# Kernel optimization log

Hardware: AMD Instinct MI355X
Metric: run time of the kernel (lower is better)

The kernel has to match this reference:

```python
import jax, jax.numpy as jnp
import numpy as np

HEADS = 8
DIM_HEAD = 32
TOP_K = 256
KMEANS_ITERS = 10
EPS_LN = 1e-6
EPS_L2 = 1e-12


def chan_layer_norm(x, gamma, beta):
    # x: (b, c, L); normalize across channel dim (biased variance)
    mean = jnp.mean(x, axis=1, keepdims=True)
    var = jnp.var(x, axis=1, keepdims=True)
    return gamma * (x - mean) / (jnp.sqrt(var) + EPS_LN) + beta


def l2norm_ch(t):
    # F.normalize(t, dim=1): L2-normalize over channel axis of (B, c, L)
    n = jnp.linalg.norm(t, axis=1, keepdims=True)
    return t / jnp.maximum(n, EPS_L2)


def conv1x1(x, w):
    # x: (b, c_in, L), w: (c_out, c_in)  -> (b, c_out, L)
    return jnp.einsum('oc,bcl->bol', w, x)


def _dist2(x, c):
    # squared L2 distances, x: (N, d), c: (k, d) -> (N, k)
    return (jnp.sum(x * x, -1, keepdims=True)
            - 2.0 * x @ c.T
            + jnp.sum(c * c, -1)[None, :])


def kmeans_fit(x, k, iters):
    # Lloyd's algorithm, deterministic init = first k points
    c0 = x[:k]

    def step(c, _):
        assign = jnp.argmin(_dist2(x, c), axis=-1)           # (N,)
        sums = jax.ops.segment_sum(x, assign, num_segments=k)
        cnts = jax.ops.segment_sum(jnp.ones((x.shape[0],), x.dtype), assign,
                                   num_segments=k)
        new_c = jnp.where(cnts[:, None] > 0,
                          sums / jnp.maximum(cnts, 1.0)[:, None], c)
        return new_c, None

    c, _ = jax.lax.scan(step, c0, None, length=iters)
    return c


def select_best_ind(q, k, v, top_k):
    # q: (B, Lq, d), k/v: (B, Lk, d); B = b*heads
    B, Lk, d = k.shape
    q_flat = q.reshape(-1, d)
    centroids = kmeans_fit(q_flat, top_k, KMEANS_ITERS)       # (top_k, d)
    k_flat = k.reshape(-1, d)
    k_cluster = jnp.argmin(_dist2(k_flat, centroids), axis=-1).reshape(B, Lk)
    k_centers = centroids[k_cluster]                          # (B, Lk, d)
    k_dist = jnp.sum(jnp.abs(k_centers - k), axis=-1)         # (B, Lk)
    _, best_k = jax.lax.top_k(k_dist, top_k)                  # largest dists
    idx = best_k[:, :, None]
    k_sel = jnp.take_along_axis(k, idx, axis=1)
    v_sel = jnp.take_along_axis(v, idx, axis=1)
    return k_sel, v_sel


def reference(query_source, context, w_q, w_kv, w_out,
              ln_ctx_gamma, ln_ctx_beta, ln_q_gamma, ln_q_beta,
              ln_out_gamma, ln_out_beta, gamma_scale):
    b, c, L_query = query_source.shape
    ctx = chan_layer_norm(context, ln_ctx_gamma, ln_ctx_beta)
    qs = chan_layer_norm(query_source, ln_q_gamma, ln_q_beta)

    kv = conv1x1(ctx, w_kv)                                   # (b, 2*inner, Lc)
    k, v = jnp.split(kv, 2, axis=1)
    q = conv1x1(qs, w_q)                                      # (b, inner, Lq)

    def fold(t):  # b (h c) L -> (b h) c L
        B, hc, L = t.shape
        return t.reshape(B, HEADS, DIM_HEAD, L).reshape(B * HEADS, DIM_HEAD, L)

    q, k, v = fold(q), fold(k), fold(v)
    q, k = l2norm_ch(q), l2norm_ch(k)
    # b d L -> b L d
    q = jnp.swapaxes(q, 1, 2)
    k = jnp.swapaxes(k, 1, 2)
    v = jnp.swapaxes(v, 1, 2)

    k, v = select_best_ind(q, k, v, TOP_K)

    sim = jnp.einsum('bid,bjd->bij', q, k)                    # (b*h, Lq, top_k)
    attn = jax.nn.softmax(sim, axis=-1)
    out = jnp.einsum('bij,bjd->bid', attn, v)                 # (b*h, Lq, dh)

    out = out.reshape(b, HEADS, L_query, DIM_HEAD)
    out = jnp.transpose(out, (0, 1, 3, 2)).reshape(b, HEADS * DIM_HEAD, L_query)
    out = conv1x1(out, w_out)
    out = chan_layer_norm(out, ln_out_gamma, ln_out_beta)
    return gamma_scale[0] * out + query_source


def setup_inputs() -> dict:
    key = jax.random.key(0)
    ks = jax.random.split(key, 8)
    dim, inner = 256, HEADS * DIM_HEAD
    b, Lq, Lc = 2, 4096, 4096
    inp = {
        'query_source': jax.random.normal(ks[0], (b, dim, Lq), jnp.float32),
        'context': jax.random.normal(ks[1], (b, dim, Lc), jnp.float32),
        'w_q': jax.random.normal(ks[2], (inner, dim), jnp.float32) * 0.05,
        'w_kv': jax.random.normal(ks[3], (2 * inner, dim), jnp.float32) * 0.05,
        'w_out': jax.random.normal(ks[4], (dim, inner), jnp.float32) * 0.05,
        'ln_ctx_gamma': jnp.ones((1, dim, 1), jnp.float32),
        'ln_ctx_beta': jnp.zeros((1, dim, 1), jnp.float32),
        'ln_q_gamma': jnp.ones((1, dim, 1), jnp.float32),
        'ln_q_beta': jnp.zeros((1, dim, 1), jnp.float32),
        'ln_out_gamma': jnp.ones((1, dim, 1), jnp.float32),
        'ln_out_beta': jnp.zeros((1, dim, 1), jnp.float32),
        'gamma_scale': jax.random.normal(ks[5], (1,), jnp.float32),
    }
    return inp
```

## Files before the change

### kernel.cpp

```cpp
#include <hip/hip_runtime.h>
#include <math.h>

#define CDIM 256
#define LSEQ 4096
#define NBH 16
#define NPTS 65536
#define KC 256

__device__ __forceinline__ float fadd(float a, float b){ return __fadd_rn(a,b); }
__device__ __forceinline__ float fmul(float a, float b){ return __fmul_rn(a,b); }
__device__ __forceinline__ float fsub(float a, float b){ return __fsub_rn(a,b); }

__device__ __forceinline__ float sum32_np(const float* e){
    float l[16];
    #pragma unroll
    for (int j = 0; j < 16; j++) l[j] = fadd(e[j], e[j + 16]);
    float t3[8];
    #pragma unroll
    for (int j = 0; j < 8; j++) t3[j] = fadd(l[j], l[j + 8]);
    float t6[4];
    #pragma unroll
    for (int j = 0; j < 4; j++) t6[j] = fadd(t3[j], t3[j + 4]);
    return fadd(fadd(t6[0], t6[2]), fadd(t6[1], t6[3]));
}

__global__ __launch_bounds__(64) void ln_np(const float* __restrict__ x,
        const float* __restrict__ g, const float* __restrict__ bt,
        float* __restrict__ y) {
    int gid = blockIdx.x * 64 + threadIdx.x;
    int b = gid >> 12, l = gid & 4095;
    const float* xb = x + (size_t)b * CDIM * LSEQ + l;
    float s = 0.f;
    #pragma unroll 8
    for (int c = 0; c < 256; c++) s = fadd(s, xb[(size_t)c * LSEQ]);
    float mean = __fdiv_rn(s, 256.f);
    float s2 = 0.f;
    #pragma unroll 8
    for (int c = 0; c < 256; c++) {
        float d = fsub(xb[(size_t)c * LSEQ], mean);
        s2 = fadd(s2, fmul(d, d));
    }
    float var = __fdiv_rn(s2, 256.f);
    float den = fadd(__fsqrt_rn(var), 1e-6f);
    float* yb = y + (size_t)b * CDIM * LSEQ + l;
    #pragma unroll 4
    for (int c = 0; c < 256; c++) {
        float d = fsub(xb[(size_t)c * LSEQ], mean);
        yb[(size_t)c * LSEQ] = fadd(__fdiv_rn(fmul(g[c], d), den), bt[c]);
    }
}

template<int COT, int NL>
__global__ __launch_bounds__(256) void conv_nl(const float* __restrict__ W, int wrow0,
        const float* __restrict__ X, float* __restrict__ Y, int nrows) {
    __shared__ float ws[COT * 256];
    int tid = threadIdx.x;
    int l0 = blockIdx.x * (256 * NL) + tid;
    int o0 = blockIdx.y * COT;
    int b = blockIdx.z;
    {
        const float4* wb4 = (const float4*)(W + (size_t)(wrow0 + o0) * CDIM);
        float4* ws4 = (float4*)ws;
        for (int i = tid; i < COT * 64; i += 256) ws4[i] = wb4[i];
    }
    __syncthreads();
    const float* xb = X + (size_t)b * CDIM * LSEQ;
    float acc[COT][NL];
    #pragma unroll
    for (int oo = 0; oo < COT; oo++)
        #pragma unroll
        for (int i = 0; i < NL; i++) acc[oo][i] = 0.f;
    const float4* ws4 = (const float4*)ws;
    for (int c = 0; c < 256; c += 4) {
        float xv[NL][4];
        #pragma unroll
        for (int i = 0; i < NL; i++) {
            #pragma unroll
            for (int k = 0; k < 4; k++)
                xv[i][k] = xb[(size_t)(c + k) * LSEQ + l0 + i * 256];
        }
        #pragma unroll
        for (int oo = 0; oo < COT; oo++) {
            float4 w = ws4[(oo * 256 + c) >> 2];
            #pragma unroll
            for (int i = 0; i < NL; i++) {
                acc[oo][i] = fadd(acc[oo][i], fmul(w.x, xv[i][0]));
                acc[oo][i] = fadd(acc[oo][i], fmul(w.y, xv[i][1]));
                acc[oo][i] = fadd(acc[oo][i], fmul(w.z, xv[i][2]));
                acc[oo][i] = fadd(acc[oo][i], fmul(w.w, xv[i][3]));
            }
        }
    }
    #pragma unroll
    for (int oo = 0; oo < COT; oo++)
        #pragma unroll
        for (int i = 0; i < NL; i++)
            Y[((size_t)b * nrows + o0 + oo) * LSEQ + l0 + i * 256] = acc[oo][i];
}

__global__ __launch_bounds__(256) void fold_np(const float* __restrict__ src,
        int srcRows, int row0, int donorm, float* __restrict__ dst,
        float* __restrict__ xxout, float* __restrict__ centout,
        float* __restrict__ ccout) {
    int p = blockIdx.x * 256 + threadIdx.x;
    int bh = p >> 12, l = p & 4095;
    int b = bh >> 3, h = bh & 7;
    const float* sp = src + ((size_t)b * srcRows + row0 + h * 32) * LSEQ + l;
    float x[32];
    #pragma unroll
    for (int t = 0; t < 32; t++) x[t] = sp[(size_t)t * LSEQ];
    float4* dp4 = (float4*)(dst + (size_t)p * 32);
    if (donorm) {
        float ss = 0.f;
        #pragma unroll
        for (int t = 0; t < 32; t++) ss = fadd(ss, fmul(x[t], x[t]));
        float n = __fsqrt_rn(ss);
        float den = fmaxf(n, 1e-12f);
        #pragma unroll
        for (int t = 0; t < 32; t++) x[t] = __fdiv_rn(x[t], den);
    }
    #pragma unroll
    for (int t = 0; t < 8; t++)
        dp4[t] = make_float4(x[4*t], x[4*t+1], x[4*t+2], x[4*t+3]);
    if (xxout) {
        float e[32];
        #pragma unroll
        for (int t = 0; t < 32; t++) e[t] = fmul(x[t], x[t]);
        float xv = sum32_np(e);
        xxout[p] = xv;
        if (centout && p < KC) {
            float4* cp4 = (float4*)(centout + (size_t)p * 32);
            #pragma unroll
            for (int t = 0; t < 8; t++)
                cp4[t] = make_float4(x[4*t], x[4*t+1], x[4*t+2], x[4*t+3]);
            ccout[p] = xv;
        }
    }
}

__global__ __launch_bounds__(256) void assign4p(const float* __restrict__ pts,
        const float* __restrict__ xx, const float* __restrict__ cent,
        const float* __restrict__ cc, int* __restrict__ asn, int* __restrict__ hist) {
    __shared__ float sc[8192];
    __shared__ float scc[256];
    __shared__ int bins[256];
    int tid = threadIdx.x, c = blockIdx.x;
    {
        const float4* c4 = (const float4*)cent;
        float4* s4 = (float4*)sc;
        for (int i = tid; i < 2048; i += 256) s4[i] = c4[i];
    }
    scc[tid] = cc[tid];
    bins[tid] = 0;
    __syncthreads();
    int pg = tid >> 2, quarter = tid & 3;
    int pb = c * 256 + pg * 4;
    float x[4][32];
    float xp[4];
    #pragma unroll
    for (int i = 0; i < 4; i++) {
        const float4* pp = (const float4*)(pts + (size_t)(pb + i) * 32);
        #pragma unroll
        for (int t = 0; t < 8; t++) {
            float4 f = pp[t];
            x[i][4*t] = f.x; x[i][4*t+1] = f.y; x[i][4*t+2] = f.z; x[i][4*t+3] = f.w;
        }
        xp[i] = xx[pb + i];
    }
    float bd[4] = {3.4e38f, 3.4e38f, 3.4e38f, 3.4e38f};
    int bj[4] = {0, 0, 0, 0};
    int jbase = quarter * 64;
    for (int jj = 0; jj < 64; jj++) {
        int j = jbase + jj;
        const float4* cj = (const float4*)(sc + j * 32);
        float w[32];
        #pragma unroll
        for (int t = 0; t < 8; t++) {
            float4 f = cj[t];
            w[4*t] = f.x; w[4*t+1] = f.y; w[4*t+2] = f.z; w[4*t+3] = f.w;
        }
        float sj = scc[j];
        #pragma unroll
        for (int i = 0; i < 4; i++) {
            float g = 0.f;
            #pragma unroll
            for (int t = 0; t < 32; t++) g = __builtin_fmaf(x[i][t], w[t], g);
            float d = fadd(fsub(xp[i], fmul(2.f, g)), sj);
            if (d < bd[i]) { bd[i] = d; bj[i] = j; }
        }
    }
    #pragma unroll
    for (int i = 0; i < 4; i++) {
        float ob; int oj;
        ob = __shfl_xor(bd[i], 1); oj = __shfl_xor(bj[i], 1);
        if (ob < bd[i]) { bd[i] = ob; bj[i] = oj; }
        ob = __shfl_xor(bd[i], 2); oj = __shfl_xor(bj[i], 2);
        if (ob < bd[i]) { bd[i] = ob; bj[i] = oj; }
    }
    if (quarter == 0) {
        #pragma unroll
        for (int i = 0; i < 4; i++) {
            asn[pb + i] = bj[i];
            atomicAdd(&bins[bj[i]], 1);
        }
    }
    __syncthreads();
    hist[c * 256 + tid] = bins[tid];
}

__global__ __launch_bounds__(256) void scan_chunks(const int* __restrict__ hist,
        int* __restrict__ chunkbase, int* __restrict__ totals) {
    __shared__ int a[256];
    int j = blockIdx.x, c = threadIdx.x;
    a[c] = hist[(size_t)c * 256 + j];
    __syncthreads();
    for (int d = 1; d < 256; d <<= 1) {
        int v = a[c];
        int u = (c >= d) ? a[c - d] : 0;
        __syncthreads();
        a[c] = v + u;
        __syncthreads();
    }
    chunkbase[(size_t)c * 256 + j] = (c == 0) ? 0 : a[c - 1];
    if (c == 255) totals[j] = a[255];
}

__global__ __launch_bounds__(256) void scatter_v5(const int* __restrict__ asn,
        const int* __restrict__ chunkbase, const int* __restrict__ totals,
        int* __restrict__ perm) {
    __shared__ int cb[256];
    __shared__ int al[256];
    int c = blockIdx.x, tid = threadIdx.x;
    cb[tid] = totals[tid];
    al[tid] = asn[c * 256 + tid];
    __syncthreads();
    for (int d = 1; d < 256; d <<= 1) {
        int v = cb[tid];
        int u = (tid >= d) ? cb[tid - d] : 0;
        __syncthreads();
        cb[tid] = v + u;
        __syncthreads();
    }
    int my = al[tid];
    int base = (my == 0) ? 0 : cb[my - 1];
    int r = 0;
    for (int i = 0; i < tid; i++) r += (al[i] == my) ? 1 : 0;
    perm[base + chunkbase[(size_t)c * 256 + my] + r] = c * 256 + tid;
}

#define STILE 128
__global__ __launch_bounds__(256) void sumk_v4(const float* __restrict__ pts,
        const int* __restrict__ perm, const int* __restrict__ totals,
        float* __restrict__ cent, float* __restrict__ cc) {
    __shared__ int cb[256];
    __shared__ float buf[2][STILE][32];
    int j = blockIdx.x, tid = threadIdx.x;
    cb[tid] = totals[tid];
    __syncthreads();
    for (int d = 1; d < 256; d <<= 1) {
        int v = cb[tid];
        int u = (tid >= d) ? cb[tid - d] : 0;
        __syncthreads();
        cb[tid] = v + u;
        __syncthreads();
    }
    int base = (j == 0) ? 0 : cb[j - 1];
    int n = totals[j];
    int t = tid & 31, r0 = tid >> 5;
    for (int r = r0; r < STILE; r += 8) {
        if (r < n) buf[0][r][t] = pts[(size_t)perm[base + r] * 32 + t];
    }
    __syncthreads();
    float s = 0.f;
    int b = 0;
    for (int i0 = 0; i0 < n; i0 += STILE, b ^= 1) {
        int nx = i0 + STILE;
        if (nx < n) {
            for (int r = r0; r < STILE; r += 8) {
                int g = nx + r;
                if (g < n) buf[b ^ 1][r][t] = pts[(size_t)perm[base + g] * 32 + t];
            }
        }
        if (tid < 32) {
            int m = n - i0; if (m > STILE) m = STILE;
            int i = 0;
            for (; i + 4 <= m; i += 4) {
                s = fadd(s, buf[b][i][tid]);
                s = fadd(s, buf[b][i + 1][tid]);
                s = fadd(s, buf[b][i + 2][tid]);
                s = fadd(s, buf[b][i + 3][tid]);
            }
            for (; i < m; i++) s = fadd(s, buf[b][i][tid]);
        }
        __syncthreads();
    }
    if (tid < 32) {
        float v;
        if (n > 0) {
            v = __fdiv_rn(s, (float)n);
            cent[(size_t)j * 32 + tid] = v;
        } else {
            v = cent[(size_t)j * 32 + tid];
        }
        float e = fmul(v, v);
        e = fadd(e, __shfl_xor(e, 16));
        e = fadd(e, __shfl_xor(e, 8));
        e = fadd(e, __shfl_xor(e, 4));
        e = fadd(e, __shfl_xor(e, 2));
        e = fadd(e, __shfl_xor(e, 1));
        if (tid == 0) cc[j] = e;
    }
}

__global__ __launch_bounds__(256) void kdist4p(const float* __restrict__ pts,
        const float* __restrict__ cent, const float* __restrict__ cc,
        float* __restrict__ kd) {
    __shared__ float sc[8192];
    __shared__ float scc[256];
    int tid = threadIdx.x, c = blockIdx.x;
    {
        const float4* c4 = (const float4*)cent;
        float4* s4 = (float4*)sc;
        for (int i = tid; i < 2048; i += 256) s4[i] = c4[i];
    }
    scc[tid] = cc[tid];
    __syncthreads();
    int pg = tid >> 2, quarter = tid & 3;
    int pb = c * 256 + pg * 4;
    float x[4][32];
    float xp[4];
    #pragma unroll
    for (int i = 0; i < 4; i++) {
        const float4* pp = (const float4*)(pts + (size_t)(pb + i) * 32);
        #pragma unroll
        for (int t = 0; t < 8; t++) {
            float4 f = pp[t];
            x[i][4*t] = f.x; x[i][4*t+1] = f.y; x[i][4*t+2] = f.z; x[i][4*t+3] = f.w;
        }
        float e[32];
        #pragma unroll
        for (int t = 0; t < 32; t++) e[t] = fmul(x[i][t], x[i][t]);
        xp[i] = sum32_np(e);
    }
    float bd[4] = {3.4e38f, 3.4e38f, 3.4e38f, 3.4e38f};
    int bj[4] = {0, 0, 0, 0};
    int jbase = quarter * 64;
    for (int jj = 0; jj < 64; jj++) {
        int j = jbase + jj;
        const float4* cj = (const float4*)(sc + j * 32);
        float w[32];
        #pragma unroll
        for (int t = 0; t < 8; t++) {
            float4 f = cj[t];
            w[4*t] = f.x; w[4*t+1] = f.y; w[4*t+2] = f.z; w[4*t+3] = f.w;
        }
        float sj = scc[j];
        #pragma unroll
        for (int i = 0; i < 4; i++) {
            float g = 0.f;
            #pragma unroll
            for (int t = 0; t < 32; t++) g = __builtin_fmaf(x[i][t], w[t], g);
            float d = fadd(fsub(xp[i], fmul(2.f, g)), sj);
            if (d < bd[i]) { bd[i] = d; bj[i] = j; }
        }
    }
    #pragma unroll
    for (int i = 0; i < 4; i++) {
        float ob; int oj;
        ob = __shfl_xor(bd[i], 1); oj = __shfl_xor(bj[i], 1);
        if (ob < bd[i]) { bd[i] = ob; bj[i] = oj; }
        ob = __shfl_xor(bd[i], 2); oj = __shfl_xor(bj[i], 2);
        if (ob < bd[i]) { bd[i] = ob; bj[i] = oj; }
    }
    if (quarter == 0) {
        #pragma unroll
        for (int i = 0; i < 4; i++) {
            const float* cb = &sc[bj[i] * 32];
            float e[32];
            #pragma unroll
            for (int t = 0; t < 32; t++) e[t] = fabsf(fsub(cb[t], x[i][t]));
            kd[pb + i] = sum32_np(e);
        }
    }
}

__global__ __launch_bounds__(256) void topk_v2(const float* __restrict__ kd,
        const float* __restrict__ k_t, const float* __restrict__ v_t,
        float* __restrict__ ksel, float* __restrict__ vsel) {
    __shared__ unsigned uv[4096];
    __shared__ int hist[256];
    __shared__ unsigned s_prefix;
    __shared__ int s_rem;
    __shared__ int sc1[256];
    __shared__ int out_src[256];
    int bh = blockIdx.x, tid = threadIdx.x;
    for (int i = tid; i < 4096; i += 256) uv[i] = __float_as_uint(kd[bh * 4096 + i]);
    if (tid == 0) { s_prefix = 0u; s_rem = 256; }
    out_src[tid] = 0;
    __syncthreads();
    for (int pass = 0; pass < 4; pass++) {
        int shift = 24 - 8 * pass;
        hist[tid] = 0;
        __syncthreads();
        unsigned pfx = s_prefix;
        for (int i = tid; i < 4096; i += 256) {
            unsigned u = uv[i];
            bool in = (pass == 0) || ((u >> (shift + 8)) == (pfx >> (shift + 8)));
            if (in) atomicAdd(&hist[(u >> shift) & 255], 1);
        }
        __syncthreads();
        if (tid == 0) {
            int rem = s_rem, cum = 0, b;
            for (b = 255; b >= 0; b--) {
                if (cum + hist[b] >= rem) break;
                cum += hist[b];
            }
            s_rem = rem - cum;
            s_prefix = s_prefix | ((unsigned)b << shift);
        }
        __syncthreads();
    }
    unsigned T = s_prefix;
    int r = s_rem;
    int base_i = tid * 16;
    int ec = 0;
    for (int q = 0; q < 16; q++) ec += (uv[base_i + q] == T) ? 1 : 0;
    sc1[tid] = ec;
    __syncthreads();
    for (int d = 1; d < 256; d <<= 1) {
        int t0 = sc1[tid];
        int u0 = (tid >= d) ? sc1[tid - d] : 0;
        __syncthreads();
        sc1[tid] = t0 + u0;
        __syncthreads();
    }
    int erank = (tid == 0) ? 0 : sc1[tid - 1];
    __syncthreads();
    bool incl[16];
    int ic = 0;
    for (int q = 0; q < 16; q++) {
        unsigned u = uv[base_i + q];
        bool inc;
        if (u > T) inc = true;
        else if (u == T) { inc = (erank < r); erank++; }
        else inc = false;
        incl[q] = inc;
        ic += inc ? 1 : 0;
    }
    sc1[tid] = ic;
    __syncthreads();
    for (int d = 1; d < 256; d <<= 1) {
        int t0 = sc1[tid];
        int u0 = (tid >= d) ? sc1[tid - d] : 0;
        __syncthreads();
        sc1[tid] = t0 + u0;
        __syncthreads();
    }
    int pos = (tid == 0) ? 0 : sc1[tid - 1];
    for (int q = 0; q < 16; q++) {
        if (incl[q]) out_src[pos++] = base_i + q;
    }
    __syncthreads();
    for (int e = tid; e < 256 * 32; e += 256) {
        int jj = e >> 5, t = e & 31;
        int src = out_src[jj];
        ksel[(size_t)bh * 8192 + e] = k_t[((size_t)bh * 4096 + src) * 32 + t];
        vsel[(size_t)bh * 8192 + e] = v_t[((size_t)bh * 4096 + src) * 32 + t];
    }
}

#define HPAD 4112
__global__ __launch_bounds__(256) void attn_v3b(const float* __restrict__ q_t,
        const float* __restrict__ ksel, const float* __restrict__ vsel,
        float* __restrict__ out) {
    __shared__ float sk[2 * HPAD];
    __shared__ float sv[2 * HPAD];
    int bh = blockIdx.y, tid = threadIdx.x;
    {
        const float4* gk = (const float4*)(ksel + (size_t)bh * 8192);
        const float4* gv = (const float4*)(vsel + (size_t)bh * 8192);
        for (int i = tid; i < 2048; i += 256) {
            int h = i >> 10, idx = i & 1023;
            ((float4*)(sk + h * HPAD))[idx] = gk[i];
            ((float4*)(sv + h * HPAD))[idx] = gv[i];
        }
    }
    __syncthreads();
    int ql = tid >> 1, slice = tid & 1;
    int p0 = bh * 4096 + blockIdx.x * 256 + ql * 2;
    float q0[32], q1[32];
    {
        const float4* qp0 = (const float4*)(q_t + (size_t)p0 * 32);
        const float4* qp1 = (const float4*)(q_t + (size_t)(p0 + 1) * 32);
        #pragma unroll
        for (int t = 0; t < 8; t++) {
            float4 f = qp0[t];
            q0[4*t] = f.x; q0[4*t+1] = f.y; q0[4*t+2] = f.z; q0[4*t+3] = f.w;
            float4 g = qp1[t];
            q1[4*t] = g.x; q1[4*t+1] = g.y; q1[4*t+2] = g.z; q1[4*t+3] = g.w;
        }
    }
    float o0[32], o1[32];
    #pragma unroll
    for (int t = 0; t < 32; t++) { o0[t] = 0.f; o1[t] = 0.f; }
    float ls0 = 0.f, ls1 = 0.f;
    const float4* k4 = (const float4*)(sk + slice * HPAD);
    const float4* v4 = (const float4*)(sv + slice * HPAD);
    for (int j = 0; j < 128; j++) {
        float a0 = 0.f, b0 = 0.f, c0 = 0.f, d0 = 0.f;
        float a1 = 0.f, b1 = 0.f, c1 = 0.f, d1 = 0.f;
        #pragma unroll
        for (int t = 0; t < 8; t++) {
            float4 kf = k4[j * 8 + t];
            a0 += q0[4*t]   * kf.x; b0 += q0[4*t+1] * kf.y;
            c0 += q0[4*t+2] * kf.z; d0 += q0[4*t+3] * kf.w;
            a1 += q1[4*t]   * kf.x; b1 += q1[4*t+1] * kf.y;
            c1 += q1[4*t+2] * kf.z; d1 += q1[4*t+3] * kf.w;
        }
        float s0 = (a0 + b0) + (c0 + d0);
        float s1 = (a1 + b1) + (c1 + d1);
        float w0 = __expf(s0 - 1.0f);
        float w1 = __expf(s1 - 1.0f);
        ls0 += w0; ls1 += w1;
        #pragma unroll
        for (int t = 0; t < 8; t++) {
            float4 vf = v4[j * 8 + t];
            o0[4*t]   += w0 * vf.x; o0[4*t+1] += w0 * vf.y;
            o0[4*t+2] += w0 * vf.z; o0[4*t+3] += w0 * vf.w;
            o1[4*t]   += w1 * vf.x; o1[4*t+1] += w1 * vf.y;
            o1[4*t+2] += w1 * vf.z; o1[4*t+3] += w1 * vf.w;
        }
    }
    #pragma unroll
    for (int t = 0; t < 32; t++) {
        o0[t] += __shfl_xor(o0[t], 1);
        o1[t] += __shfl_xor(o1[t], 1);
    }
    ls0 += __shfl_xor(ls0, 1);
    ls1 += __shfl_xor(ls1, 1);
    if (slice == 0) {
        float inv0 = 1.f / ls0, inv1 = 1.f / ls1;
        float4* op0 = (float4*)(out + (size_t)p0 * 32);
        float4* op1 = (float4*)(out + (size_t)(p0 + 1) * 32);
        #pragma unroll
        for (int t = 0; t < 8; t++) {
            op0[t] = make_float4(o0[4*t]*inv0, o0[4*t+1]*inv0, o0[4*t+2]*inv0, o0[4*t+3]*inv0);
            op1[t] = make_float4(o1[4*t]*inv1, o1[4*t+1]*inv1, o1[4*t+2]*inv1, o1[4*t+3]*inv1);
        }
    }
}

__global__ __launch_bounds__(256) void unfold_kernel(const float* __restrict__ att,
        float* __restrict__ Fo) {
    __shared__ float tbuf[32][65];
    int bh = blockIdx.y, l0 = blockIdx.x * 64;
    int b = bh >> 3, h = bh & 7;
    int tid = threadIdx.x;
    #pragma unroll
    for (int r = 0; r < 8; r++) {
        int e = r * 256 + tid;
        int l = e >> 5, d = e & 31;
        tbuf[d][l] = att[((size_t)bh * 4096 + l0 + l) * 32 + d];
    }
    __syncthreads();
    #pragma unroll
    for (int r = 0; r < 8; r++) {
        int e = r * 256 + tid;
        int d = e >> 6, l = e & 63;
        Fo[((size_t)b * 256 + h * 32 + d) * LSEQ + l0 + l] = tbuf[d][l];
    }
}

__global__ __launch_bounds__(64) void lnres_np(const float* __restrict__ x,
        const float* __restrict__ g, const float* __restrict__ bt,
        const float* __restrict__ gs, const float* __restrict__ qsrc,
        float* __restrict__ y) {
    int gid = blockIdx.x * 64 + threadIdx.x;
    int b = gid >> 12, l = gid & 4095;
    const float* xb = x + (size_t)b * CDIM * LSEQ + l;
    float s = 0.f;
    #pragma unroll 8
    for (int c = 0; c < 256; c++) s = fadd(s, xb[(size_t)c * LSEQ]);
    float mean = __fdiv_rn(s, 256.f);
    float s2 = 0.f;
    #pragma unroll 8
    for (int c = 0; c < 256; c++) {
        float d = fsub(xb[(size_t)c * LSEQ], mean);
        s2 = fadd(s2, fmul(d, d));
    }
    float var = __fdiv_rn(s2, 256.f);
    float den = fadd(__fsqrt_rn(var), 1e-6f);
    float scale = gs[0];
    const float* qb = qsrc + (size_t)b * CDIM * LSEQ + l;
    float* yb = y + (size_t)b * CDIM * LSEQ + l;
    #pragma unroll 4
    for (int c = 0; c < 256; c++) {
        float d = fsub(xb[(size_t)c * LSEQ], mean);
        float r = fadd(__fdiv_rn(fmul(g[c], d), den), bt[c]);
        yb[(size_t)c * LSEQ] = fadd(fmul(scale, r), qb[(size_t)c * LSEQ]);
    }
}

extern "C" void kernel_launch(void* const* d_in, const int* in_sizes, int n_in,
                              void* d_out, int out_size, void* d_ws, size_t ws_size,
                              hipStream_t stream) {
    const float* qsrc   = (const float*)d_in[0];
    const float* ctx    = (const float*)d_in[1];
    const float* w_q    = (const float*)d_in[2];
    const float* w_kv   = (const float*)d_in[3];
    const float* w_out  = (const float*)d_in[4];
    const float* g_ctx  = (const float*)d_in[5];
    const float* b_ctx  = (const float*)d_in[6];
    const float* g_q    = (const float*)d_in[7];
    const float* b_q    = (const float*)d_in[8];
    const float* g_out  = (const float*)d_in[9];
    const float* b_out  = (const float*)d_in[10];
    const float* gs     = (const float*)d_in[11];

    char* base = (char*)d_ws;
    const size_t MB = 1024 * 1024;
    float* yln   = (float*)base;
    float* att   = (float*)base;
    float* kvbuf = (float*)(base + 8 * MB);
    float* y32   = (float*)(base + 8 * MB);
    float* qbuf  = (float*)(base + 24 * MB);
    float* Fo    = (float*)(base + 24 * MB);
    float* q_t   = (float*)(base + 32 * MB);
    float* k_t   = (float*)(base + 40 * MB);
    float* v_t   = (float*)(base + 48 * MB);
    char* SM = base + 56 * MB;
    float* xx_q      = (float*)(SM + 0);
    float* cent      = (float*)(SM + 512 * 1024);
    float* cc        = (float*)(SM + 576 * 1024);
    int*   totals    = (int*)  (SM + 640 * 1024);
    int*   asn       = (int*)  (SM + 704 * 1024);
    int*   hist      = (int*)  (SM + 960 * 1024);
    int*   chunkbase = (int*)  (SM + 1472 * 1024);
    int*   perm      = (int*)  (SM + 1984 * 1024);
    float* kd        = (float*)(SM + 2240 * 1024);
    float* ksel      = (float*)(SM + 2496 * 1024);
    float* vsel      = (float*)(SM + 3008 * 1024);

    ln_np<<<128, 64, 0, stream>>>(ctx, g_ctx, b_ctx, yln);
    conv_nl<16, 2><<<dim3(8, 32, 2), 256, 0, stream>>>(w_kv, 0, yln, kvbuf, 512);
    fold_np<<<256, 256, 0, stream>>>(kvbuf, 512, 0, 1, k_t, nullptr, nullptr, nullptr);
    fold_np<<<256, 256, 0, stream>>>(kvbuf, 512, 256, 0, v_t, nullptr, nullptr, nullptr);
    ln_np<<<128, 64, 0, stream>>>(qsrc, g_q, b_q, yln);
    conv_nl<8, 2><<<dim3(8, 32, 2), 256, 0, stream>>>(w_q, 0, yln, qbuf, 256);
    fold_np<<<256, 256, 0, stream>>>(qbuf, 256, 0, 1, q_t, xx_q, cent, cc);

    for (int it = 0; it < 10; it++) {
        assign4p<<<256, 256, 0, stream>>>(q_t, xx_q, cent, cc, asn, hist);
        scan_chunks<<<256, 256, 0, stream>>>(hist, chunkbase, totals);
        scatter_v5<<<256, 256, 0, stream>>>(asn, chunkbase, totals, perm);
        sumk_v4<<<256, 256, 0, stream>>>(q_t, perm, totals, cent, cc);
    }

    kdist4p<<<256, 256, 0, stream>>>(k_t, cent, cc, kd);
    topk_v2<<<16, 256, 0, stream>>>(kd, k_t, v_t, ksel, vsel);
    attn_v3b<<<dim3(16, 16), 256, 0, stream>>>(q_t, ksel, vsel, att);
    unfold_kernel<<<dim3(64, 16), 256, 0, stream>>>(att, Fo);
    conv_nl<8, 2><<<dim3(8, 32, 2), 256, 0, stream>>>(w_out, 0, Fo, y32, 256);
    lnres_np<<<128, 64, 0, stream>>>(y32, g_out, b_out, gs, qsrc, (float*)d_out);
}
```

Baseline: 977.9 us.

## Merge layernorms and folds, use FMA convs for V/out, split attention head dim

The two layer norms now run in one launch writing to separate buffers, and the three fold launches become one. The V half of the KV projection and the output projection switch to fused multiply-add accumulation, while K keeps exact separate rounding because it feeds k-means selection. Attention moves to 512 threads, with each query pair's head dimension split across two lanes and partial dot products combined by a shuffle. The goal is fewer launches and more parallelism in attention, at the cost of small rounding differences in V and the output path.

New measurement: 969.3 us. About the same (-0.9%).

```diff
diff --git a/kernel.cpp b/kernel.cpp
--- a/kernel.cpp
+++ b/kernel.cpp
@@ -24,11 +24,19 @@
     return fadd(fadd(t6[0], t6[2]), fadd(t6[1], t6[3]));
 }
 
-__global__ __launch_bounds__(64) void ln_np(const float* __restrict__ x,
-        const float* __restrict__ g, const float* __restrict__ bt,
-        float* __restrict__ y) {
+__global__ __launch_bounds__(64) void ln2_np(
+        const float* __restrict__ x0, const float* __restrict__ g0,
+        const float* __restrict__ bt0, float* __restrict__ y0,
+        const float* __restrict__ x1, const float* __restrict__ g1,
+        const float* __restrict__ bt1, float* __restrict__ y1) {
     int gid = blockIdx.x * 64 + threadIdx.x;
-    int b = gid >> 12, l = gid & 4095;
+    int which = gid >> 13;
+    int r = gid & 8191;
+    int b = r >> 12, l = r & 4095;
+    const float* x  = which ? x1 : x0;
+    const float* g  = which ? g1 : g0;
+    const float* bt = which ? bt1 : bt0;
+    float* y        = which ? y1 : y0;
     const float* xb = x + (size_t)b * CDIM * LSEQ + l;
     float s = 0.f;
     #pragma unroll 8
@@ -51,7 +59,7 @@
 }
 
 template<int COT, int NL>
-__global__ __launch_bounds__(256) void conv_nl(const float* __restrict__ W, int wrow0,
+__global__ __launch_bounds__(256) void conv_nl(const float* __restrict__ W, int row0,
         const float* __restrict__ X, float* __restrict__ Y, int nrows) {
     __shared__ float ws[COT * 256];
     int tid = threadIdx.x;
@@ -59,7 +67,7 @@
     int o0 = blockIdx.y * COT;
     int b = blockIdx.z;
     {
-        const float4* wb4 = (const float4*)(W + (size_t)(wrow0 + o0) * CDIM);
+        const float4* wb4 = (const float4*)(W + (size_t)(row0 + o0) * CDIM);
         float4* ws4 = (float4*)ws;
         for (int i = tid; i < COT * 64; i += 256) ws4[i] = wb4[i];
     }
@@ -95,14 +103,61 @@
     for (int oo = 0; oo < COT; oo++)
         #pragma unroll
         for (int i = 0; i < NL; i++)
-            Y[((size_t)b * nrows + o0 + oo) * LSEQ + l0 + i * 256] = acc[oo][i];
-}
-
-__global__ __launch_bounds__(256) void fold_np(const float* __restrict__ src,
+            Y[((size_t)b * nrows + row0 + o0 + oo) * LSEQ + l0 + i * 256] = acc[oo][i];
+}
+
+template<int COT, int NL>
+__global__ __launch_bounds__(256) void conv_fma(const float* __restrict__ W, int row0,
+        const float* __restrict__ X, float* __restrict__ Y, int nrows) {
+    __shared__ float ws[COT * 256];
+    int tid = threadIdx.x;
+    int l0 = blockIdx.x * (256 * NL) + tid;
+    int o0 = blockIdx.y * COT;
+    int b = blockIdx.z;
+    {
+        const float4* wb4 = (const float4*)(W + (size_t)(row0 + o0) * CDIM);
+        float4* ws4 = (float4*)ws;
+        for (int i = tid; i < COT * 64; i += 256) ws4[i] = wb4[i];
+    }
+    __syncthreads();
+    const float* xb = X + (size_t)b * CDIM * LSEQ;
+    float acc[COT][NL];
+    #pragma unroll
+    for (int oo = 0; oo < COT; oo++)
+        #pragma unroll
+        for (int i = 0; i < NL; i++) acc[oo][i] = 0.f;
+    const float4* ws4 = (const float4*)ws;
+    for (int c = 0; c < 256; c += 4) {
+        float xv[NL][4];
+        #pragma unroll
+        for (int i = 0; i < NL; i++) {
+            #pragma unroll
+            for (int k = 0; k < 4; k++)
+                xv[i][k] = xb[(size_t)(c + k) * LSEQ + l0 + i * 256];
+        }
+        #pragma unroll
+        for (int oo = 0; oo < COT; oo++) {
+            float4 w = ws4[(oo * 256 + c) >> 2];
+            #pragma unroll
+            for (int i = 0; i < NL; i++) {
+                acc[oo][i] = __builtin_fmaf(w.x, xv[i][0], acc[oo][i]);
+                acc[oo][i] = __builtin_fmaf(w.y, xv[i][1], acc[oo][i]);
+                acc[oo][i] = __builtin_fmaf(w.z, xv[i][2], acc[oo][i]);
+                acc[oo][i] = __builtin_fmaf(w.w, xv[i][3], acc[oo][i]);
+            }
+        }
+    }
+    #pragma unroll
+    for (int oo = 0; oo < COT; oo++)
+        #pragma unroll
+        for (int i = 0; i < NL; i++)
+            Y[((size_t)b * nrows + row0 + o0 + oo) * LSEQ + l0 + i * 256] = acc[oo][i];
+}
+
+__device__ __forceinline__ void fold_body(const float* __restrict__ src,
         int srcRows, int row0, int donorm, float* __restrict__ dst,
         float* __restrict__ xxout, float* __restrict__ centout,
-        float* __restrict__ ccout) {
-    int p = blockIdx.x * 256 + threadIdx.x;
+        float* __restrict__ ccout, int p) {
     int bh = p >> 12, l = p & 4095;
     int b = bh >> 3, h = bh & 7;
     const float* sp = src + ((size_t)b * srcRows + row0 + h * 32) * LSEQ + l;
@@ -135,6 +190,20 @@
                 cp4[t] = make_float4(x[4*t], x[4*t+1], x[4*t+2], x[4*t+3]);
             ccout[p] = xv;
         }
+    }
+}
+
+__global__ __launch_bounds__(256) void fold3_np(const float* __restrict__ kvbuf,
+        const float* __restrict__ qbuf, float* __restrict__ k_t,
+        float* __restrict__ v_t, float* __restrict__ q_t,
+        float* __restrict__ xx, float* __restrict__ cent, float* __restrict__ cc) {
+    int blk = blockIdx.x, tid = threadIdx.x;
+    if (blk < 256) {
+        fold_body(kvbuf, 512, 0, 1, k_t, nullptr, nullptr, nullptr, blk * 256 + tid);
+    } else if (blk < 512) {
+        fold_body(kvbuf, 512, 256, 0, v_t, nullptr, nullptr, nullptr, (blk - 256) * 256 + tid);
+    } else {
+        fold_body(qbuf, 256, 0, 1, q_t, xx, cent, cc, (blk - 512) * 256 + tid);
     }
 }
 
@@ -470,7 +539,7 @@
 }
 
 #define HPAD 4112
-__global__ __launch_bounds__(256) void attn_v3b(const float* __restrict__ q_t,
+__global__ __launch_bounds__(512) void attn_v3c(const float* __restrict__ q_t,
         const float* __restrict__ ksel, const float* __restrict__ vsel,
         float* __restrict__ out) {
     __shared__ float sk[2 * HPAD];
@@ -479,52 +548,56 @@
     {
         const float4* gk = (const float4*)(ksel + (size_t)bh * 8192);
         const float4* gv = (const float4*)(vsel + (size_t)bh * 8192);
-        for (int i = tid; i < 2048; i += 256) {
+        for (int i = tid; i < 2048; i += 512) {
             int h = i >> 10, idx = i & 1023;
             ((float4*)(sk + h * HPAD))[idx] = gk[i];
             ((float4*)(sv + h * HPAD))[idx] = gv[i];
         }
     }
     __syncthreads();
-    int ql = tid >> 1, slice = tid & 1;
-    int p0 = bh * 4096 + blockIdx.x * 256 + ql * 2;
-    float q0[32], q1[32];
+    int grp = tid >> 2;
+    int slice = tid & 1;
+    int dh = (tid >> 1) & 1;
+    int p0 = bh * 4096 + blockIdx.x * 256 + grp * 2;
+    float q0[16], q1[16];
     {
-        const float4* qp0 = (const float4*)(q_t + (size_t)p0 * 32);
-        const float4* qp1 = (const float4*)(q_t + (size_t)(p0 + 1) * 32);
-        #pragma unroll
-        for (int t = 0; t < 8; t++) {
+        const float4* qp0 = (const float4*)(q_t + (size_t)p0 * 32 + dh * 16);
+        const float4* qp1 = (const float4*)(q_t + (size_t)(p0 + 1) * 32 + dh * 16);
+        #pragma unroll
+        for (int t = 0; t < 4; t++) {
             float4 f = qp0[t];
             q0[4*t] = f.x; q0[4*t+1] = f.y; q0[4*t+2] = f.z; q0[4*t+3] = f.w;
             float4 g = qp1[t];
             q1[4*t] = g.x; q1[4*t+1] = g.y; q1[4*t+2] = g.z; q1[4*t+3] = g.w;
         }
     }
-    float o0[32], o1[32];
-    #pragma unroll
-    for (int t = 0; t < 32; t++) { o0[t] = 0.f; o1[t] = 0.f; }
+    float o0[16], o1[16];
+    #pragma unroll
+    for (int t = 0; t < 16; t++) { o0[t] = 0.f; o1[t] = 0.f; }
     float ls0 = 0.f, ls1 = 0.f;
-    const float4* k4 = (const float4*)(sk + slice * HPAD);
-    const float4* v4 = (const float4*)(sv + slice * HPAD);
+    const float* kb = sk + slice * HPAD + dh * 16;
+    const float* vb = sv + slice * HPAD + dh * 16;
     for (int j = 0; j < 128; j++) {
         float a0 = 0.f, b0 = 0.f, c0 = 0.f, d0 = 0.f;
         float a1 = 0.f, b1 = 0.f, c1 = 0.f, d1 = 0.f;
         #pragma unroll
-        for (int t = 0; t < 8; t++) {
-            float4 kf = k4[j * 8 + t];
+        for (int t = 0; t < 4; t++) {
+            float4 kf = *(const float4*)(kb + j * 32 + t * 4);
             a0 += q0[4*t]   * kf.x; b0 += q0[4*t+1] * kf.y;
             c0 += q0[4*t+2] * kf.z; d0 += q0[4*t+3] * kf.w;
             a1 += q1[4*t]   * kf.x; b1 += q1[4*t+1] * kf.y;
             c1 += q1[4*t+2] * kf.z; d1 += q1[4*t+3] * kf.w;
         }
-        float s0 = (a0 + b0) + (c0 + d0);
-        float s1 = (a1 + b1) + (c1 + d1);
-        float w0 = __expf(s0 - 1.0f);
-        float w1 = __expf(s1 - 1.0f);
+        float ps0 = (a0 + b0) + (c0 + d0);
+        float ps1 = (a1 + b1) + (c1 + d1);
+        ps0 += __shfl_xor(ps0, 2);
+        ps1 += __shfl_xor(ps1, 2);
+        float w0 = __expf(ps0 - 1.0f);
+        float w1 = __expf(ps1 - 1.0f);
         ls0 += w0; ls1 += w1;
         #pragma unroll
-        for (int t = 0; t < 8; t++) {
-            float4 vf = v4[j * 8 + t];
+        for (int t = 0; t < 4; t++) {
+            float4 vf = *(const float4*)(vb + j * 32 + t * 4);
             o0[4*t]   += w0 * vf.x; o0[4*t+1] += w0 * vf.y;
             o0[4*t+2] += w0 * vf.z; o0[4*t+3] += w0 * vf.w;
             o1[4*t]   += w1 * vf.x; o1[4*t+1] += w1 * vf.y;
@@ -532,7 +605,7 @@
         }
     }
     #pragma unroll
-    for (int t = 0; t < 32; t++) {
+    for (int t = 0; t < 16; t++) {
         o0[t] += __shfl_xor(o0[t], 1);
         o1[t] += __shfl_xor(o1[t], 1);
     }
@@ -540,10 +613,10 @@
     ls1 += __shfl_xor(ls1, 1);
     if (slice == 0) {
         float inv0 = 1.f / ls0, inv1 = 1.f / ls1;
-        float4* op0 = (float4*)(out + (size_t)p0 * 32);
-        float4* op1 = (float4*)(out + (size_t)(p0 + 1) * 32);
-        #pragma unroll
-        for (int t = 0; t < 8; t++) {
+        float4* op0 = (float4*)(out + (size_t)p0 * 32 + dh * 16);
+        float4* op1 = (float4*)(out + (size_t)(p0 + 1) * 32 + dh * 16);
+        #pragma unroll
+        for (int t = 0; t < 4; t++) {
             op0[t] = make_float4(o0[4*t]*inv0, o0[4*t+1]*inv0, o0[4*t+2]*inv0, o0[4*t+3]*inv0);
             op1[t] = make_float4(o1[4*t]*inv1, o1[4*t+1]*inv1, o1[4*t+2]*inv1, o1[4*t+3]*inv1);
         }
@@ -640,14 +713,14 @@
     float* kd        = (float*)(SM + 2240 * 1024);
     float* ksel      = (float*)(SM + 2496 * 1024);
     float* vsel      = (float*)(SM + 3008 * 1024);
-
-    ln_np<<<128, 64, 0, stream>>>(ctx, g_ctx, b_ctx, yln);
-    conv_nl<16, 2><<<dim3(8, 32, 2), 256, 0, stream>>>(w_kv, 0, yln, kvbuf, 512);
-    fold_np<<<256, 256, 0, stream>>>(kvbuf, 512, 0, 1, k_t, nullptr, nullptr, nullptr);
-    fold_np<<<256, 256, 0, stream>>>(kvbuf, 512, 256, 0, v_t, nullptr, nullptr, nullptr);
-    ln_np<<<128, 64, 0, stream>>>(qsrc, g_q, b_q, yln);
-    conv_nl<8, 2><<<dim3(8, 32, 2), 256, 0, stream>>>(w_q, 0, yln, qbuf, 256);
-    fold_np<<<256, 256, 0, stream>>>(qbuf, 256, 0, 1, q_t, xx_q, cent, cc);
+    float* yln_q     = (float*)(base + 60 * MB);
+
+    ln2_np<<<256, 64, 0, stream>>>(ctx, g_ctx, b_ctx, yln,
+                                   qsrc, g_q, b_q, yln_q);
+    conv_nl<16, 2><<<dim3(8, 16, 2), 256, 0, stream>>>(w_kv, 0, yln, kvbuf, 512);
+    conv_fma<16, 2><<<dim3(8, 16, 2), 256, 0, stream>>>(w_kv, 256, yln, kvbuf, 512);
+    conv_nl<8, 2><<<dim3(8, 32, 2), 256, 0, stream>>>(w_q, 0, yln_q, qbuf, 256);
+    fold3_np<<<768, 256, 0, stream>>>(kvbuf, qbuf, k_t, v_t, q_t, xx_q, cent, cc);
 
     for (int it = 0; it < 10; it++) {
         assign4p<<<256, 256, 0, stream>>>(q_t, xx_q, cent, cc, asn, hist);
@@ -658,8 +731,8 @@
 
     kdist4p<<<256, 256, 0, stream>>>(k_t, cent, cc, kd);
     topk_v2<<<16, 256, 0, stream>>>(kd, k_t, v_t, ksel, vsel);
-    attn_v3b<<<dim3(16, 16), 256, 0, stream>>>(q_t, ksel, vsel, att);
+    attn_v3c<<<dim3(16, 16), 512, 0, stream>>>(q_t, ksel, vsel, att);
     unfold_kernel<<<dim3(64, 16), 256, 0, stream>>>(att, Fo);
-    conv_nl<8, 2><<<dim3(8, 32, 2), 256, 0, stream>>>(w_out, 0, Fo, y32, 256);
+    conv_fma<8, 2><<<dim3(8, 32, 2), 256, 0, stream>>>(w_out, 0, Fo, y32, 256);
     lnres_np<<<128, 64, 0, stream>>>(y32, g_out, b_out, gs, qsrc, (float*)d_out);
 }
```
